# Performance work log

Measured on AMD Instinct MI355X. Metric: run time of the kernel, lower is better.

## Reference

```python
import math
import jax, jax.numpy as jnp
import numpy as np


def setup_inputs() -> dict:
    key = jax.random.key(0)
    k1, k2, k3 = jax.random.split(key, 3)
    B, N, D = 8192, 64, 128
    return {
        "x_t": jax.random.normal(k1, (B, D), dtype=jnp.float32),
        "means": jax.random.normal(k2, (N, D), dtype=jnp.float32),
        "cholesky_factors": jax.random.normal(k3, (N, D, D), dtype=jnp.float32),
    }


def reference(x_t, means, cholesky_factors):
    # x_t: (B, D), means: (N, D), cholesky_factors: (N, D, D)
    N, D = means.shape
    log_c = D * math.log(2.0 * math.pi)

    # tril + exp-reparameterized diagonal
    L_tril = jnp.tril(cholesky_factors)                      # (N, D, D)
    eye = jnp.eye(D, dtype=bool)
    L = jnp.where(eye, jnp.exp(L_tril), L_tril)              # (N, D, D)

    # log det Sigma = 2 * sum(log diag(L)); diag(L) = exp(raw diag)
    diag_raw = jnp.diagonal(L_tril, axis1=-2, axis2=-1)      # (N, D)
    log_det_Sigma = 2.0 * jnp.sum(diag_raw, axis=-1)         # (N,)

    # delta[b, n, :] = x_t[b] - means[n]
    delta = x_t[:, None, :] - means[None, :, :]              # (B, N, D)

    # Solve L y = delta per state, batching B into the RHS columns
    # (avoids materializing L expanded over the batch).
    rhs = jnp.transpose(delta, (1, 2, 0))                    # (N, D, B)
    y = jax.scipy.linalg.solve_triangular(L, rhs, lower=True)  # (N, D, B)
    quad = jnp.transpose(jnp.sum(y * y, axis=1))             # (B, N)

    log_p = -0.5 * (log_c + log_det_Sigma[None, :] + quad)   # (B, N)
    return log_p
```

## Files before the change

kernel.cpp:

```cpp
#include <hip/hip_runtime.h>
#include <math.h>

#define DD 128
#define BB 8192
#define NN 64
#define LOGC 235.24826450039622f
#define CLAMP_M 1.0e12f
#define YCLAMP 1.0e18f
#define KP 136
#define PITCH 129

typedef __attribute__((ext_vector_type(8))) short bf16x8;
typedef __attribute__((ext_vector_type(4))) float f32x4;

__device__ __forceinline__ unsigned int f2bf(float x) {
    unsigned int u = __float_as_uint(x);
    return (u + 0x7FFFu + ((u >> 16) & 1u)) >> 16;
}
__device__ __forceinline__ unsigned int pack2(float lo, float hi) {
    return f2bf(lo) | (f2bf(hi) << 16);
}
__device__ __forceinline__ float clampM(float x) {
    return fminf(fmaxf(x, -CLAMP_M), CLAMP_M);
}
__device__ __forceinline__ float lane_bcast(float v, int j) {
    return __int_as_float(__builtin_amdgcn_readlane(__float_as_int(v), j));
}

__global__ __launch_bounds__(256, 2)
void solve_columns(const float* __restrict__ chol,
                   const float* __restrict__ means,
                   unsigned short* __restrict__ Mout,
                   float* __restrict__ vout,
                   float* __restrict__ termout)
{
    const int n = blockIdx.y;
    const int grp = blockIdx.x;
    const int t = threadIdx.x;
    const int lane = t & 63;
    const int w = t >> 6;
    const float* __restrict__ Ln = chol + (size_t)n * DD * DD;

    const bool is_mu = (grp == 4);
    const int jmin = is_mu ? 0 : grp * 32;

    __shared__ float LsT[DD][PITCH];
    __shared__ float s_invd[DD];
    __shared__ float s_raw[DD];

    #pragma unroll
    for (int it = 0; it < 16; ++it) {
        const int id = it * 256 + t;
        const int i = id >> 5;
        const int j0 = (id & 31) * 4;
        if (j0 < jmin) continue;
        if (i <= j0) {
            LsT[j0 + 0][i] = 0.0f;
            LsT[j0 + 1][i] = 0.0f;
            LsT[j0 + 2][i] = 0.0f;
            LsT[j0 + 3][i] = 0.0f;
        } else {
            const float4 vv = *(const float4*)(Ln + (size_t)i * DD + j0);
            LsT[j0 + 0][i] = (i > j0 + 0) ? vv.x : 0.0f;
            LsT[j0 + 1][i] = (i > j0 + 1) ? vv.y : 0.0f;
            LsT[j0 + 2][i] = (i > j0 + 2) ? vv.z : 0.0f;
            LsT[j0 + 3][i] = (i > j0 + 3) ? vv.w : 0.0f;
        }
    }
    if (t < DD) {
        const float raw = Ln[(size_t)t * DD + t];
        s_raw[t] = raw;
        s_invd[t] = __expf(-raw);
    }
    __syncthreads();

    if (is_mu) {
        if (w == 0) {
            float rl = means[(size_t)n * DD + lane];
            float rh = means[(size_t)n * DD + 64 + lane];
            #pragma unroll 4
            for (int j = 0; j < 64; ++j) {
                const float y = clampM(lane_bcast(rl, j) * s_invd[j]);
                rl = fmaf(-LsT[j][lane], y, rl);
                rh = fmaf(-LsT[j][64 + lane], y, rh);
            }
            #pragma unroll 4
            for (int j = 64; j < 128; ++j) {
                const float y = clampM(lane_bcast(rh, j - 64) * s_invd[j]);
                rh = fmaf(-LsT[j][64 + lane], y, rh);
            }
            vout[(size_t)n * DD + lane] = clampM(rl * s_invd[lane]);
            vout[(size_t)n * DD + 64 + lane] = clampM(rh * s_invd[64 + lane]);
        } else if (w == 1) {
            float v = s_raw[lane] + s_raw[64 + lane];
            #pragma unroll
            for (int o = 32; o > 0; o >>= 1) v += __shfl_down(v, o);
            if (lane == 0) termout[n] = LOGC + 2.0f * v;
        }
        return;
    }

    const int c0 = grp * 32 + w * 8;
    float rl[8], rh[8];
    #pragma unroll
    for (int ch = 0; ch < 8; ++ch) {
        rl[ch] = (lane == c0 + ch) ? 1.0f : 0.0f;
        rh[ch] = (lane + 64 == c0 + ch) ? 1.0f : 0.0f;
    }

    #pragma unroll 2
    for (int j = c0; j < 64; ++j) {
        const float invd = s_invd[j];
        const float Ll = LsT[j][lane];
        const float Lh = LsT[j][64 + lane];
        float yv[8];
        #pragma unroll
        for (int ch = 0; ch < 8; ++ch)
            yv[ch] = clampM(lane_bcast(rl[ch], j) * invd);
        #pragma unroll
        for (int ch = 0; ch < 8; ++ch) {
            rl[ch] = fmaf(-Ll, yv[ch], rl[ch]);
            rh[ch] = fmaf(-Lh, yv[ch], rh[ch]);
        }
    }
    #pragma unroll 2
    for (int j = (c0 > 64 ? c0 : 64); j < 128; ++j) {
        const float invd = s_invd[j];
        const float Lh = LsT[j][64 + lane];
        float yv[8];
        #pragma unroll
        for (int ch = 0; ch < 8; ++ch)
            yv[ch] = clampM(lane_bcast(rh[ch], j - 64) * invd);
        #pragma unroll
        for (int ch = 0; ch < 8; ++ch)
            rh[ch] = fmaf(-Lh, yv[ch], rh[ch]);
    }

    const float i_lo = s_invd[lane], i_hi = s_invd[64 + lane];
    float ylo[8], yhi[8];
    #pragma unroll
    for (int ch = 0; ch < 8; ++ch) {
        ylo[ch] = clampM(rl[ch] * i_lo);
        yhi[ch] = clampM(rh[ch] * i_hi);
    }
    uint4 plo, phi;
    plo.x = pack2(ylo[0], ylo[1]); plo.y = pack2(ylo[2], ylo[3]);
    plo.z = pack2(ylo[4], ylo[5]); plo.w = pack2(ylo[6], ylo[7]);
    phi.x = pack2(yhi[0], yhi[1]); phi.y = pack2(yhi[2], yhi[3]);
    phi.z = pack2(yhi[4], yhi[5]); phi.w = pack2(yhi[6], yhi[7]);
    *(uint4*)&Mout[((size_t)n * DD + lane) * DD + c0] = plo;
    *(uint4*)&Mout[((size_t)n * DD + 64 + lane) * DD + c0] = phi;
}

__global__ __launch_bounds__(256, 2)
void emission_mfma(const float* __restrict__ x,
                   const unsigned short* __restrict__ Mws,
                   const float* __restrict__ vws,
                   const float* __restrict__ termws,
                   float* __restrict__ out)
{
    const int btile = blockIdx.x;
    const int ngrp = blockIdx.y;
    const int t = threadIdx.x;
    const int lane = t & 63;
    const int w = t >> 6;
    const int wi = w >> 1;
    const int wb = w & 1;

    __shared__ __align__(16) unsigned short xs[128 * KP];
    __shared__ __align__(16) unsigned short as[128 * KP];
    __shared__ __align__(16) float sv[DD];
    __shared__ float sterm[8];
    __shared__ float redbuf[2 * 128];
    __shared__ float qbuf[8 * 128];

    const int bbase = btile * 128;

    #pragma unroll
    for (int it = 0; it < 8; ++it) {
        const int id = it * 256 + t;
        const int brow = id >> 4;
        const int koff = (id & 15) * 8;
        const float4* px = (const float4*)(x + (size_t)(bbase + brow) * DD + koff);
        const float4 a = px[0], b = px[1];
        uint4 p;
        p.x = pack2(a.x, a.y);
        p.y = pack2(a.z, a.w);
        p.z = pack2(b.x, b.y);
        p.w = pack2(b.z, b.w);
        *(uint4*)&xs[brow * KP + koff] = p;
    }
    __syncthreads();

    bf16x8 bf[4][4];
    #pragma unroll
    for (int bt = 0; bt < 4; ++bt)
        #pragma unroll
        for (int ks = 0; ks < 4; ++ks) {
            const int col = wb * 64 + bt * 16 + (lane & 15);
            const int k = ks * 32 + (lane >> 4) * 8;
            bf[bt][ks] = *(const bf16x8*)&xs[col * KP + k];
        }

    const f32x4 zero = {0.0f, 0.0f, 0.0f, 0.0f};

    for (int nl = 0; nl < 8; ++nl) {
        const int n = ngrp * 8 + nl;
        const unsigned short* __restrict__ Mn = Mws + (size_t)n * DD * DD;
        #pragma unroll
        for (int it = 0; it < 8; ++it) {
            const int id = it * 256 + t;
            const int row = id >> 4;
            const int koff = (id & 15) * 8;
            *(uint4*)&as[row * KP + koff] = *(const uint4*)&Mn[row * DD + koff];
        }
        if (t < DD) sv[t] = vws[n * DD + t];
        if (t == 0) sterm[nl] = termws[n];
        if (nl > 0 && t < 128) qbuf[(nl - 1) * 128 + t] = redbuf[t] + redbuf[128 + t];
        __syncthreads();

        f32x4 acc[4][4];
        #pragma unroll
        for (int it = 0; it < 4; ++it)
            #pragma unroll
            for (int bt = 0; bt < 4; ++bt) acc[it][bt] = zero;

        #pragma unroll
        for (int ks = 0; ks < 4; ++ks) {
            bf16x8 af[4];
            #pragma unroll
            for (int it = 0; it < 4; ++it) {
                const int row = wi * 64 + it * 16 + (lane & 15);
                const int k = ks * 32 + (lane >> 4) * 8;
                af[it] = *(const bf16x8*)&as[row * KP + k];
            }
            #pragma unroll
            for (int it = 0; it < 4; ++it)
                #pragma unroll
                for (int bt = 0; bt < 4; ++bt)
                    acc[it][bt] = __builtin_amdgcn_mfma_f32_16x16x32_bf16(
                        af[it], bf[bt][ks], acc[it][bt], 0, 0, 0);
        }

        float p[4] = {0.0f, 0.0f, 0.0f, 0.0f};
        #pragma unroll
        for (int it = 0; it < 4; ++it) {
            const int rowbase = wi * 64 + it * 16 + (lane >> 4) * 4;
            const f32x4 v4 = *(const f32x4*)&sv[rowbase];
            #pragma unroll
            for (int bt = 0; bt < 4; ++bt) {
                const f32x4 a = acc[it][bt];
                const float t0 = a.x - v4.x, t1 = a.y - v4.y;
                const float t2 = a.z - v4.z, t3 = a.w - v4.w;
                p[bt] += t0 * t0 + t1 * t1 + t2 * t2 + t3 * t3;
            }
        }
        #pragma unroll
        for (int bt = 0; bt < 4; ++bt) {
            float pv = p[bt];
            pv += __shfl_xor(pv, 16);
            pv += __shfl_xor(pv, 32);
            if (lane < 16) redbuf[wi * 128 + wb * 64 + bt * 16 + lane] = pv;
        }
        __syncthreads();
    }

    if (t < 128) {
        qbuf[7 * 128 + t] = redbuf[t] + redbuf[128 + t];
        float o[8];
        #pragma unroll
        for (int j = 0; j < 8; ++j)
            o[j] = -0.5f * (sterm[j] + qbuf[j * 128 + t]);
        float* po = &out[(size_t)(bbase + t) * NN + ngrp * 8];
        *(float4*)&po[0] = make_float4(o[0], o[1], o[2], o[3]);
        *(float4*)&po[4] = make_float4(o[4], o[5], o[6], o[7]);
    }
}

__global__ __launch_bounds__(256, 2)
void emission_solve_fb(const float* __restrict__ xin,
                       const float* __restrict__ means,
                       const float* __restrict__ chol,
                       float* __restrict__ out)
{
    const int n = blockIdx.y;
    const int t = threadIdx.x;
    const int b = blockIdx.x * 256 + t;
    const float* __restrict__ Ln = chol + (size_t)n * DD * DD;

    __shared__ float s_invd[DD];
    __shared__ float s_mu[DD];
    __shared__ float s_part[4];

    float raw = 0.0f;
    if (t < DD) {
        raw = Ln[t * DD + t];
        s_invd[t] = 1.0f / expf(raw);
        s_mu[t] = means[n * DD + t];
    }
    float v = raw;
    #pragma unroll
    for (int o = 32; o > 0; o >>= 1) v += __shfl_down(v, o);
    if ((t & 63) == 0) s_part[t >> 6] = v;
    __syncthreads();

    const float term = LOGC + 2.0f * (s_part[0] + s_part[1] + s_part[2] + s_part[3]);

    float y[DD];
    float quad = 0.0f;
    #pragma unroll
    for (int i = 0; i < DD; ++i) {
        const float xv = xin[(size_t)b * DD + i] - s_mu[i];
        float sA = 0.0f, sB = 0.0f;
        #pragma unroll
        for (int j = 0; j + 1 < i; j += 2) {
            sA = fmaf(Ln[i * DD + j], y[j], sA);
            sB = fmaf(Ln[i * DD + j + 1], y[j + 1], sB);
        }
        if (i & 1) sA = fmaf(Ln[i * DD + (i - 1)], y[i - 1], sA);
        const float s = xv - sA - sB;
        float yi = s * s_invd[i];
        yi = fminf(fmaxf(yi, -YCLAMP), YCLAMP);
        y[i] = yi;
        quad = fmaf(yi, yi, quad);
    }
    out[(size_t)b * NN + n] = -0.5f * (term + quad);
}

extern "C" void kernel_launch(void* const* d_in, const int* in_sizes, int n_in,
                              void* d_out, int out_size, void* d_ws, size_t ws_size,
                              hipStream_t stream) {
    const float* x     = (const float*)d_in[0];
    const float* means = (const float*)d_in[1];
    const float* chol  = (const float*)d_in[2];
    float* out = (float*)d_out;

    const size_t needM = (size_t)NN * DD * DD * sizeof(unsigned short);
    const size_t needV = (size_t)NN * DD * sizeof(float);
    const size_t needT = (size_t)NN * sizeof(float);

    if (ws_size >= needM + needV + needT) {
        unsigned short* Mws = (unsigned short*)d_ws;
        float* vws = (float*)((char*)d_ws + needM);
        float* tws = (float*)((char*)d_ws + needM + needV);
        solve_columns<<<dim3(5, NN), 256, 0, stream>>>(chol, means, Mws, vws, tws);
        emission_mfma<<<dim3(BB / 128, 8), 256, 0, stream>>>(x, Mws, vws, tws, out);
    } else {
        emission_solve_fb<<<dim3(BB / 256, NN), 256, 0, stream>>>(x, means, chol, out);
    }
}
```

Measured before the change: 107.2 us.

## Halve batch tile in MFMA emission kernel and reuse shared buffer

Batch tile per block goes from 128 to 64 rows, doubling the grid. The x tile and M tile now share one LDS buffer since x is kept in registers after loading. Per-wave accumulators shrink from 4x4 to 2x4, the launch-bounds occupancy hint rises from 2 to 3, all 8 v vectors are preloaded, and the reduction buffer is double-buffered. The aim is more resident blocks and less LDS per block. The cost is that each M matrix is loaded from global memory twice as many times overall, lowering reuse per load.

```diff
diff --git a/kernel.cpp b/kernel.cpp
--- a/kernel.cpp
+++ b/kernel.cpp
@@ -4,6 +4,7 @@
 #define DD 128
 #define BB 8192
 #define NN 64
+#define BT 64
 #define LOGC 235.24826450039622f
 #define CLAMP_M 1.0e12f
 #define YCLAMP 1.0e18f
@@ -152,7 +153,7 @@
     *(uint4*)&Mout[((size_t)n * DD + 64 + lane) * DD + c0] = phi;
 }
 
-__global__ __launch_bounds__(256, 2)
+__global__ __launch_bounds__(256, 3)
 void emission_mfma(const float* __restrict__ x,
                    const unsigned short* __restrict__ Mws,
                    const float* __restrict__ vws,
@@ -164,20 +165,17 @@
     const int t = threadIdx.x;
     const int lane = t & 63;
     const int w = t >> 6;
-    const int wi = w >> 1;
-    const int wb = w & 1;
-
-    __shared__ __align__(16) unsigned short xs[128 * KP];
-    __shared__ __align__(16) unsigned short as[128 * KP];
-    __shared__ __align__(16) float sv[DD];
+
+    __shared__ __align__(16) unsigned short Ms[128 * KP];
+    __shared__ __align__(16) float sv8[8 * DD];
+    __shared__ float qbuf[8 * BT];
+    __shared__ float redbuf[2][4 * BT];
     __shared__ float sterm[8];
-    __shared__ float redbuf[2 * 128];
-    __shared__ float qbuf[8 * 128];
-
-    const int bbase = btile * 128;
-
-    #pragma unroll
-    for (int it = 0; it < 8; ++it) {
+
+    const int bbase = btile * BT;
+
+    #pragma unroll
+    for (int it = 0; it < 4; ++it) {
         const int id = it * 256 + t;
         const int brow = id >> 4;
         const int koff = (id & 15) * 8;
@@ -188,8 +186,10 @@
         p.y = pack2(a.z, a.w);
         p.z = pack2(b.x, b.y);
         p.w = pack2(b.z, b.w);
-        *(uint4*)&xs[brow * KP + koff] = p;
-    }
+        *(uint4*)&Ms[brow * KP + koff] = p;
+    }
+    *(float4*)&sv8[4 * t] = *(const float4*)&vws[(size_t)ngrp * 8 * DD + 4 * t];
+    if (t < 8) sterm[t] = termws[ngrp * 8 + t];
     __syncthreads();
 
     bf16x8 bf[4][4];
@@ -197,45 +197,47 @@
     for (int bt = 0; bt < 4; ++bt)
         #pragma unroll
         for (int ks = 0; ks < 4; ++ks) {
-            const int col = wb * 64 + bt * 16 + (lane & 15);
+            const int col = bt * 16 + (lane & 15);
             const int k = ks * 32 + (lane >> 4) * 8;
-            bf[bt][ks] = *(const bf16x8*)&xs[col * KP + k];
-        }
+            bf[bt][ks] = *(const bf16x8*)&Ms[col * KP + k];
+        }
+    __syncthreads();
 
     const f32x4 zero = {0.0f, 0.0f, 0.0f, 0.0f};
 
     for (int nl = 0; nl < 8; ++nl) {
-        const int n = ngrp * 8 + nl;
-        const unsigned short* __restrict__ Mn = Mws + (size_t)n * DD * DD;
+        const unsigned short* __restrict__ Mn =
+            Mws + (size_t)(ngrp * 8 + nl) * DD * DD;
         #pragma unroll
         for (int it = 0; it < 8; ++it) {
             const int id = it * 256 + t;
             const int row = id >> 4;
             const int koff = (id & 15) * 8;
-            *(uint4*)&as[row * KP + koff] = *(const uint4*)&Mn[row * DD + koff];
-        }
-        if (t < DD) sv[t] = vws[n * DD + t];
-        if (t == 0) sterm[nl] = termws[n];
-        if (nl > 0 && t < 128) qbuf[(nl - 1) * 128 + t] = redbuf[t] + redbuf[128 + t];
+            *(uint4*)&Ms[row * KP + koff] = *(const uint4*)&Mn[row * DD + koff];
+        }
+        if (nl > 0 && t < BT) {
+            const float* rb = redbuf[(nl - 1) & 1];
+            qbuf[(nl - 1) * BT + t] = rb[t] + rb[BT + t] + rb[2 * BT + t] + rb[3 * BT + t];
+        }
         __syncthreads();
 
-        f32x4 acc[4][4];
-        #pragma unroll
-        for (int it = 0; it < 4; ++it)
+        f32x4 acc[2][4];
+        #pragma unroll
+        for (int it = 0; it < 2; ++it)
             #pragma unroll
             for (int bt = 0; bt < 4; ++bt) acc[it][bt] = zero;
 
         #pragma unroll
         for (int ks = 0; ks < 4; ++ks) {
-            bf16x8 af[4];
-            #pragma unroll
-            for (int it = 0; it < 4; ++it) {
-                const int row = wi * 64 + it * 16 + (lane & 15);
+            bf16x8 af[2];
+            #pragma unroll
+            for (int it = 0; it < 2; ++it) {
+                const int row = w * 32 + it * 16 + (lane & 15);
                 const int k = ks * 32 + (lane >> 4) * 8;
-                af[it] = *(const bf16x8*)&as[row * KP + k];
+                af[it] = *(const bf16x8*)&Ms[row * KP + k];
             }
             #pragma unroll
-            for (int it = 0; it < 4; ++it)
+            for (int it = 0; it < 2; ++it)
                 #pragma unroll
                 for (int bt = 0; bt < 4; ++bt)
                     acc[it][bt] = __builtin_amdgcn_mfma_f32_16x16x32_bf16(
@@ -244,9 +246,9 @@
 
         float p[4] = {0.0f, 0.0f, 0.0f, 0.0f};
         #pragma unroll
-        for (int it = 0; it < 4; ++it) {
-            const int rowbase = wi * 64 + it * 16 + (lane >> 4) * 4;
-            const f32x4 v4 = *(const f32x4*)&sv[rowbase];
+        for (int it = 0; it < 2; ++it) {
+            const int rowbase = w * 32 + it * 16 + (lane >> 4) * 4;
+            const f32x4 v4 = *(const f32x4*)&sv8[nl * DD + rowbase];
             #pragma unroll
             for (int bt = 0; bt < 4; ++bt) {
                 const f32x4 a = acc[it][bt];
@@ -255,22 +257,24 @@
                 p[bt] += t0 * t0 + t1 * t1 + t2 * t2 + t3 * t3;
             }
         }
+        float* rb = redbuf[nl & 1];
         #pragma unroll
         for (int bt = 0; bt < 4; ++bt) {
             float pv = p[bt];
             pv += __shfl_xor(pv, 16);
             pv += __shfl_xor(pv, 32);
-            if (lane < 16) redbuf[wi * 128 + wb * 64 + bt * 16 + lane] = pv;
+            if (lane < 16) rb[w * BT + bt * 16 + lane] = pv;
         }
         __syncthreads();
     }
 
-    if (t < 128) {
-        qbuf[7 * 128 + t] = redbuf[t] + redbuf[128 + t];
+    if (t < BT) {
+        const float* rb = redbuf[1];
+        qbuf[7 * BT + t] = rb[t] + rb[BT + t] + rb[2 * BT + t] + rb[3 * BT + t];
         float o[8];
         #pragma unroll
         for (int j = 0; j < 8; ++j)
-            o[j] = -0.5f * (sterm[j] + qbuf[j * 128 + t]);
+            o[j] = -0.5f * (sterm[j] + qbuf[j * BT + t]);
         float* po = &out[(size_t)(bbase + t) * NN + ngrp * 8];
         *(float4*)&po[0] = make_float4(o[0], o[1], o[2], o[3]);
         *(float4*)&po[4] = make_float4(o[4], o[5], o[6], o[7]);
@@ -344,7 +348,7 @@
         float* vws = (float*)((char*)d_ws + needM);
         float* tws = (float*)((char*)d_ws + needM + needV);
         solve_columns<<<dim3(5, NN), 256, 0, stream>>>(chol, means, Mws, vws, tws);
-        emission_mfma<<<dim3(BB / 128, 8), 256, 0, stream>>>(x, Mws, vws, tws, out);
+        emission_mfma<<<dim3(BB / BT, 8), 256, 0, stream>>>(x, Mws, vws, tws, out);
     } else {
         emission_solve_fb<<<dim3(BB / 256, NN), 256, 0, stream>>>(x, means, chol, out);
     }
```

Result: slower. 113.4 us (+5.8%).
